# Kernel tuning notes

Measured on AMD Instinct MI355X. Metric: run time of the kernel, lower is better.

Reference implementation:

```python
import jax, jax.numpy as jnp
import numpy as np


def setup_inputs() -> dict:
    key = jax.random.key(0)
    ks = jax.random.split(key, 5)
    B, DEC, ENC, H = 4, 256, 256, 512  # feature_dim = hl_size = 512, mlp hidden = 512
    decoder_states = jax.random.normal(ks[0], (B, DEC, H), dtype=jnp.float32)
    encoder_states = jax.random.normal(ks[1], (B, ENC, H), dtype=jnp.float32)
    ext_mask = jnp.zeros((B, DEC, ENC), dtype=bool)  # self.mask set externally; all-False here
    W_mlp = jax.random.normal(ks[2], (2 * H, H), dtype=jnp.float32) * 0.02  # Linear(2H -> H)
    b_mlp = jnp.zeros((H,), dtype=jnp.float32)
    W_out = jax.random.normal(ks[3], (H, 1), dtype=jnp.float32) * 0.02  # Linear(H -> 1)
    b_out = jnp.zeros((1,), dtype=jnp.float32)
    return {"decoder_states": decoder_states, "encoder_states": encoder_states,
            "ext_mask": ext_mask, "W_mlp": W_mlp, "b_mlp": b_mlp,
            "W_out": W_out, "b_out": b_out}


def reference(decoder_states, encoder_states, ext_mask, W_mlp, b_mlp, W_out, b_out):
    # decoder_states: [B, dec, H]; encoder_states: [B, enc, H]
    H = encoder_states.shape[-1]
    # pad mask: positions where encoder feature-0 equals 0.0 -> [B, 1, enc]
    pad_mask = (encoder_states == 0.0)[:, :, :1]
    pad_mask = jnp.swapaxes(pad_mask, 1, 2)  # [B, 1, enc]
    # cat(enc, dec) @ W_mlp  ==  enc @ W_mlp[:H] + dec @ W_mlp[H:]  (avoids 2H concat)
    enc_proj = jnp.einsum('beh,hm->bem', encoder_states, W_mlp[:H])   # [B, enc, Hm]
    dec_proj = jnp.einsum('bdh,hm->bdm', decoder_states, W_mlp[H:])   # [B, dec, Hm]
    hidden = jnp.tanh(dec_proj[:, :, None, :] + enc_proj[:, None, :, :] + b_mlp)  # [B, dec, enc, Hm]
    attn = jnp.einsum('bdem,mo->bde', hidden, W_out) + b_out[0]       # [B, dec, enc]
    attn = jnp.where(ext_mask, -jnp.inf, attn)
    attn = jnp.where(pad_mask, -jnp.inf, attn)
    attn = jax.nn.softmax(attn, axis=-1)
    context = jnp.einsum('bde,beh->bdh', attn, encoder_states)        # [B, dec, H]
    return (context, attn)
```

## Files before the change

kernel.cpp:

```cpp
#include <hip/hip_runtime.h>
#include <math.h>

#define B 4
#define DEC 256
#define ENC 256
#define HDIM 512

#define TANH_SCALE 2.8853900817779268f
#define LOG2E 1.4426950408889634f

__device__ __forceinline__ float fast_exp2(float x) { return __builtin_amdgcn_exp2f(x); }
__device__ __forceinline__ float fast_rcp(float x)  { return __builtin_amdgcn_rcpf(x); }

typedef __attribute__((ext_vector_type(8))) short bf16x8;
typedef __attribute__((ext_vector_type(4))) short bf16x4;
typedef __attribute__((ext_vector_type(4))) float f32x4;

__device__ __forceinline__ unsigned short bf16_rne(float x) {
    unsigned u = __float_as_uint(x);
    return (unsigned short)((u + 0x7FFFu + ((u >> 16) & 1u)) >> 16);
}
__device__ __forceinline__ float bf16_to_f(unsigned short h) {
    return __uint_as_float((unsigned)h << 16);
}

#define W_OFS(m, k) ((((long)(m) >> 4) << 13) + (((long)(k) >> 3) << 7) + (((m) & 15) << 3) + ((k) & 7))

__global__ __launch_bounds__(256) void convert_kernel(
    const float* __restrict__ enc, const float* __restrict__ dec,
    const float* __restrict__ Wmlp,
    unsigned short* __restrict__ Xh_e, unsigned short* __restrict__ Xl_e,
    unsigned short* __restrict__ Xh_d, unsigned short* __restrict__ Xl_d,
    unsigned short* __restrict__ Wh_e, unsigned short* __restrict__ Wl_e,
    unsigned short* __restrict__ Wh_d, unsigned short* __restrict__ Wl_d)
{
    const int tid = threadIdx.x, z = blockIdx.z;
    if (z < 2) {
        const float* X = z ? dec : enc;
        unsigned short* H = z ? Xh_d : Xh_e;
        unsigned short* L = z ? Xl_d : Xl_e;
        const long i8 = ((long)blockIdx.x * 256 + tid) * 8;
        float4 v0 = *(const float4*)(X + i8);
        float4 v1 = *(const float4*)(X + i8 + 4);
        float xs[8] = {v0.x, v0.y, v0.z, v0.w, v1.x, v1.y, v1.z, v1.w};
        bf16x8 hv, lv;
#pragma unroll
        for (int j = 0; j < 8; ++j) {
            unsigned short h = bf16_rne(xs[j]);
            hv[j] = (short)h;
            lv[j] = (short)bf16_rne(xs[j] - bf16_to_f(h));
        }
        *(bf16x8*)(H + i8) = hv;
        *(bf16x8*)(L + i8) = lv;
    } else {
        const float* Wsrc = Wmlp + (z == 3 ? (long)HDIM * HDIM : 0);
        unsigned short* H = (z == 3) ? Wh_d : Wh_e;
        unsigned short* L = (z == 3) ? Wl_d : Wl_e;
        const int t = blockIdx.x * 256 + tid;
        const int m = t & 511;
        const int k0 = (t >> 9) << 2;
        bf16x4 hv, lv;
#pragma unroll
        for (int j = 0; j < 4; ++j) {
            float x = Wsrc[(long)(k0 + j) * 512 + m];
            unsigned short h = bf16_rne(x);
            hv[j] = (short)h;
            lv[j] = (short)bf16_rne(x - bf16_to_f(h));
        }
        const long ofs = W_OFS(m, k0);
        *(bf16x4*)(H + ofs) = hv;
        *(bf16x4*)(L + ofs) = lv;
    }
}

__global__ __launch_bounds__(256) void proj_mfma_kernel(
    const unsigned short* __restrict__ Xh_e, const unsigned short* __restrict__ Xl_e,
    const unsigned short* __restrict__ Xh_d, const unsigned short* __restrict__ Xl_d,
    const unsigned short* __restrict__ Wh_e, const unsigned short* __restrict__ Wl_e,
    const unsigned short* __restrict__ Wh_d, const unsigned short* __restrict__ Wl_d,
    const float* __restrict__ bmlp,
    float* __restrict__ ET, float* __restrict__ Dmat)
{
    const int tid = threadIdx.x;
    const int wave = tid >> 6, lane = tid & 63;
    const int z = blockIdx.z;
    const int r0w = blockIdx.x * 64 + wave * 16;
    const int m0 = blockIdx.y * 32;
    const unsigned short* Xh = z ? Xh_d : Xh_e;
    const unsigned short* Xl = z ? Xl_d : Xl_e;
    const unsigned short* Wh = z ? Wh_d : Wh_e;
    const unsigned short* Wl = z ? Wl_d : Wl_e;

    const int col = lane & 15;
    const int quad = lane >> 4;

    const unsigned short* pah = Xh + (long)(r0w + col) * 512 + quad * 8;
    const unsigned short* pal = Xl + (long)(r0w + col) * 512 + quad * 8;
    const long bofs = ((long)(m0 >> 4) << 13) + (quad << 7) + (col << 3);
    const unsigned short* pb0h = Wh + bofs;
    const unsigned short* pb0l = Wl + bofs;
    const unsigned short* pb1h = Wh + bofs + 8192;
    const unsigned short* pb1l = Wl + bofs + 8192;

    f32x4 a0h = {0.f,0.f,0.f,0.f}, a0x = {0.f,0.f,0.f,0.f};
    f32x4 a1h = {0.f,0.f,0.f,0.f}, a1x = {0.f,0.f,0.f,0.f};

    bf16x8 Ah = *(const bf16x8*)pah,  Al = *(const bf16x8*)pal;
    bf16x8 B0h = *(const bf16x8*)pb0h, B0l = *(const bf16x8*)pb0l;
    bf16x8 B1h = *(const bf16x8*)pb1h, B1l = *(const bf16x8*)pb1l;

#pragma unroll 1
    for (int k0 = 0; k0 < 512; k0 += 32) {
        bf16x8 nAh = Ah, nAl = Al, nB0h = B0h, nB0l = B0l, nB1h = B1h, nB1l = B1l;
        if (k0 + 32 < 512) {
            nAh = *(const bf16x8*)(pah + k0 + 32);
            nAl = *(const bf16x8*)(pal + k0 + 32);
            const long ko = (long)(k0 + 32) << 4;
            nB0h = *(const bf16x8*)(pb0h + ko);
            nB0l = *(const bf16x8*)(pb0l + ko);
            nB1h = *(const bf16x8*)(pb1h + ko);
            nB1l = *(const bf16x8*)(pb1l + ko);
        }
        a0h = __builtin_amdgcn_mfma_f32_16x16x32_bf16(Ah, B0h, a0h, 0, 0, 0);
        a1h = __builtin_amdgcn_mfma_f32_16x16x32_bf16(Ah, B1h, a1h, 0, 0, 0);
        a0x = __builtin_amdgcn_mfma_f32_16x16x32_bf16(Ah, B0l, a0x, 0, 0, 0);
        a1x = __builtin_amdgcn_mfma_f32_16x16x32_bf16(Ah, B1l, a1x, 0, 0, 0);
        a0x = __builtin_amdgcn_mfma_f32_16x16x32_bf16(Al, B0h, a0x, 0, 0, 0);
        a1x = __builtin_amdgcn_mfma_f32_16x16x32_bf16(Al, B1h, a1x, 0, 0, 0);
        Ah = nAh; Al = nAl; B0h = nB0h; B0l = nB0l; B1h = nB1h; B1l = nB1l;
    }

    if (z == 0) {
        const int batch = r0w >> 8;
        const int e0 = (r0w & 255) + quad * 4;
        float* base = ET + (long)batch * HDIM * ENC;
        float4 v;
        v.x = fast_exp2((a0h[0] + a0x[0]) * TANH_SCALE);
        v.y = fast_exp2((a0h[1] + a0x[1]) * TANH_SCALE);
        v.z = fast_exp2((a0h[2] + a0x[2]) * TANH_SCALE);
        v.w = fast_exp2((a0h[3] + a0x[3]) * TANH_SCALE);
        *(float4*)&base[(long)(m0 + col) * ENC + e0] = v;
        v.x = fast_exp2((a1h[0] + a1x[0]) * TANH_SCALE);
        v.y = fast_exp2((a1h[1] + a1x[1]) * TANH_SCALE);
        v.z = fast_exp2((a1h[2] + a1x[2]) * TANH_SCALE);
        v.w = fast_exp2((a1h[3] + a1x[3]) * TANH_SCALE);
        *(float4*)&base[(long)(m0 + 16 + col) * ENC + e0] = v;
    } else {
        const float bq0 = bmlp[m0 + col];
        const float bq1 = bmlp[m0 + 16 + col];
        const int r = r0w + quad * 4;
#pragma unroll
        for (int i = 0; i < 4; ++i) {
            Dmat[(long)(r + i) * HDIM + m0 + col] =
                fast_exp2((a0h[i] + a0x[i] + bq0) * TANH_SCALE);
            Dmat[(long)(r + i) * HDIM + m0 + 16 + col] =
                fast_exp2((a1h[i] + a1x[i] + bq1) * TANH_SCALE);
        }
    }
}

__global__ __launch_bounds__(512) void attn_ctx_kernel(
    const float* __restrict__ Dmat, const float* __restrict__ ET,
    const float* __restrict__ wo,
    const float* __restrict__ enc, const unsigned char* __restrict__ extm,
    float* __restrict__ attn_out, float* __restrict__ ctx)
{
    __shared__ __align__(16) float ds[4][HDIM];
    __shared__ __align__(16) float wos[HDIM];
    __shared__ __align__(16) float pbuf[8][4][ENC];
    __shared__ __align__(16) float as4T[ENC][4];
    __shared__ float redm[4][4];
    __shared__ float reds[4][4];

    const int tid = threadIdx.x;
    const int b = blockIdx.z, d0 = blockIdx.x * 4;
    const long g0 = (long)b * DEC + d0;
    const int rot = blockIdx.x >> 3;

    ((float4*)ds)[tid] = ((const float4*)(Dmat + g0 * HDIM))[tid];
    if (tid < 128) ((float4*)wos)[tid] = ((const float4*)wo)[tid];

    const int mg = ((tid >> 6) + rot) & 7;
    const int e4 = (tid & 63) * 4;
    const int mbase = mg * 64;
    const float* ep = ET + (long)b * HDIM * ENC + (long)mbase * ENC + e4;

    float4 rb[8];
#pragma unroll
    for (int j = 0; j < 8; ++j) rb[j] = *(const float4*)(ep + (long)j * ENC);
    __syncthreads();

    float acc[4][4] = {};
    for (int i = 0; i < 64; i += 4) {
        float4 c0 = rb[0], c1 = rb[1], c2 = rb[2], c3 = rb[3];
        rb[0] = rb[4]; rb[1] = rb[5]; rb[2] = rb[6]; rb[3] = rb[7];
        if (i + 8 < 64) {
#pragma unroll
            for (int j = 0; j < 4; ++j)
                rb[4 + j] = *(const float4*)(ep + (long)(i + 8 + j) * ENC);
        }
        const int m = mbase + i;
        const float4 w4 = *(const float4*)&wos[m];
#pragma unroll
        for (int r = 0; r < 4; ++r) {
            const float4 d4 = *(const float4*)&ds[r][m];
#pragma unroll
            for (int j = 0; j < 4; ++j) {
                acc[r][j] = fmaf(w4.x, fast_rcp(fmaf(((const float*)&c0)[j], d4.x, 1.0f)), acc[r][j]);
                acc[r][j] = fmaf(w4.y, fast_rcp(fmaf(((const float*)&c1)[j], d4.y, 1.0f)), acc[r][j]);
                acc[r][j] = fmaf(w4.z, fast_rcp(fmaf(((const float*)&c2)[j], d4.z, 1.0f)), acc[r][j]);
                acc[r][j] = fmaf(w4.w, fast_rcp(fmaf(((const float*)&c3)[j], d4.w, 1.0f)), acc[r][j]);
            }
        }
    }
#pragma unroll
    for (int r = 0; r < 4; ++r) {
        float4 v = make_float4(acc[r][0], acc[r][1], acc[r][2], acc[r][3]);
        *(float4*)&pbuf[mg][r][e4] = v;
    }
    __syncthreads();

    const int ty = tid >> 8;
    const int e = tid & 255;
    const int wave = tid >> 6, lane = tid & 63;

    const bool pad = (enc[((long)b * ENC + e) * HDIM] == 0.0f);
    float l[2], p[2];
#pragma unroll
    for (int rl = 0; rl < 2; ++rl) {
        const int r = ty * 2 + rl;
        float a = 0.f;
#pragma unroll
        for (int q = 0; q < 8; ++q) a += pbuf[q][r][e];
        const bool xm = extm[(g0 + r) * ENC + e] != 0;
        l[rl] = (pad || xm) ? -__builtin_inff() : -2.0f * a;
    }
    float mx[2] = {l[0], l[1]};
#pragma unroll
    for (int off = 32; off >= 1; off >>= 1) {
#pragma unroll
        for (int rl = 0; rl < 2; ++rl)
            mx[rl] = fmaxf(mx[rl], __shfl_xor(mx[rl], off, 64));
    }
    if (lane == 0) {
        redm[ty * 2 + 0][wave & 3] = mx[0];
        redm[ty * 2 + 1][wave & 3] = mx[1];
    }
    __syncthreads();
    float s[2];
#pragma unroll
    for (int rl = 0; rl < 2; ++rl) {
        const int r = ty * 2 + rl;
        const float gm = fmaxf(fmaxf(redm[r][0], redm[r][1]),
                               fmaxf(redm[r][2], redm[r][3]));
        p[rl] = fast_exp2((l[rl] - gm) * LOG2E);
        s[rl] = p[rl];
    }
#pragma unroll
    for (int off = 32; off >= 1; off >>= 1) {
#pragma unroll
        for (int rl = 0; rl < 2; ++rl)
            s[rl] += __shfl_xor(s[rl], off, 64);
    }
    if (lane == 0) {
        reds[ty * 2 + 0][wave & 3] = s[0];
        reds[ty * 2 + 1][wave & 3] = s[1];
    }
    __syncthreads();
#pragma unroll
    for (int rl = 0; rl < 2; ++rl) {
        const int r = ty * 2 + rl;
        const float gs = reds[r][0] + reds[r][1] + reds[r][2] + reds[r][3];
        const float pr = p[rl] * fast_rcp(gs);
        attn_out[(g0 + r) * ENC + e] = pr;
        as4T[e][r] = pr;
    }
    __syncthreads();

    float (*p4c)[4][HDIM] = (float (*)[4][HDIM])pbuf;

    const int hq = (tid & 127) * 4;
    const int eq = ((tid >> 7) + rot) & 3;
    const int ebase = eq * 64;
    const float* ew = enc + (long)b * ENC * HDIM + (long)ebase * HDIM + hq;

    float4 wb[8];
#pragma unroll
    for (int j = 0; j < 8; ++j) wb[j] = *(const float4*)(ew + (long)j * HDIM);

    float a4[4][4] = {};
    for (int i = 0; i < 64; i += 4) {
        float4 c0 = wb[0], c1 = wb[1], c2 = wb[2], c3 = wb[3];
        wb[0] = wb[4]; wb[1] = wb[5]; wb[2] = wb[6]; wb[3] = wb[7];
        if (i + 8 < 64) {
#pragma unroll
            for (int j = 0; j < 4; ++j)
                wb[4 + j] = *(const float4*)(ew + (long)(i + 8 + j) * HDIM);
        }
        float4 pa = *(const float4*)&as4T[ebase + i][0];
        float4 pb = *(const float4*)&as4T[ebase + i + 1][0];
        float4 pc = *(const float4*)&as4T[ebase + i + 2][0];
        float4 pd = *(const float4*)&as4T[ebase + i + 3][0];
#pragma unroll
        for (int r = 0; r < 4; ++r) {
            const float par = ((const float*)&pa)[r];
            const float pbr = ((const float*)&pb)[r];
            const float pcr = ((const float*)&pc)[r];
            const float pdr = ((const float*)&pd)[r];
#pragma unroll
            for (int j = 0; j < 4; ++j) {
                a4[r][j] = fmaf(par, ((const float*)&c0)[j], a4[r][j]);
                a4[r][j] = fmaf(pbr, ((const float*)&c1)[j], a4[r][j]);
                a4[r][j] = fmaf(pcr, ((const float*)&c2)[j], a4[r][j]);
                a4[r][j] = fmaf(pdr, ((const float*)&c3)[j], a4[r][j]);
            }
        }
    }
#pragma unroll
    for (int r = 0; r < 4; ++r)
        *(float4*)&p4c[eq][r][hq] = make_float4(a4[r][0], a4[r][1], a4[r][2], a4[r][3]);
    __syncthreads();

    const int h = tid;
#pragma unroll
    for (int r = 0; r < 4; ++r) {
        const float o = p4c[0][r][h] + p4c[1][r][h] + p4c[2][r][h] + p4c[3][r][h];
        ctx[(g0 + r) * HDIM + h] = o;
    }
}

extern "C" void kernel_launch(void* const* d_in, const int* in_sizes, int n_in,
                              void* d_out, int out_size, void* d_ws, size_t ws_size,
                              hipStream_t stream) {
    const float* dec = (const float*)d_in[0];
    const float* enc = (const float*)d_in[1];
    const unsigned char* extm = (const unsigned char*)d_in[2];
    const float* Wmlp = (const float*)d_in[3];
    const float* bmlp = (const float*)d_in[4];
    const float* Wout = (const float*)d_in[5];

    float* ctx = (float*)d_out;
    float* attn = ctx + (size_t)B * DEC * HDIM;

    const size_t F = (size_t)B * DEC * HDIM;
    float* ET = (float*)d_ws;
    float* Dmat = ET + F;
    unsigned short* Xh_e = (unsigned short*)(Dmat + F);
    unsigned short* Xl_e = Xh_e + F;
    unsigned short* Xh_d = Xl_e + F;
    unsigned short* Xl_d = Xh_d + F;
    unsigned short* Wh_e = Xl_d + F;
    unsigned short* Wl_e = Wh_e + HDIM * HDIM;
    unsigned short* Wh_d = Wl_e + HDIM * HDIM;
    unsigned short* Wl_d = Wh_d + HDIM * HDIM;

    convert_kernel<<<dim3(256, 1, 4), 256, 0, stream>>>(
        enc, dec, Wmlp, Xh_e, Xl_e, Xh_d, Xl_d, Wh_e, Wl_e, Wh_d, Wl_d);
    proj_mfma_kernel<<<dim3(16, 16, 2), 256, 0, stream>>>(
        Xh_e, Xl_e, Xh_d, Xl_d, Wh_e, Wl_e, Wh_d, Wl_d, bmlp, ET, Dmat);
    attn_ctx_kernel<<<dim3(DEC / 4, 1, B), 512, 0, stream>>>(
        Dmat, ET, Wout, enc, extm, attn, ctx);
}
```

Before: 108.4 us.

## Fuse convert, projection and attention kernels into one cooperative kernel

Merges the three launches (bf16 split conversion, MFMA projection, attention/softmax/context) into a single cooperative kernel of 256 blocks by 512 threads, separated by grid-wide syncs. Work of each former kernel is remapped onto the fixed block count: the conversion does two items per thread, and the projection packs two old 256-thread tiles per block. The goal is to remove launch gaps between kernels. In exchange it adds grid-sync overhead, and the projection phase now runs on 256 blocks of 512 threads instead of 512 blocks of 256.

```diff
diff --git a/kernel.cpp b/kernel.cpp
--- a/kernel.cpp
+++ b/kernel.cpp
@@ -1,5 +1,8 @@
 #include <hip/hip_runtime.h>
+#include <hip/hip_cooperative_groups.h>
 #include <math.h>
+
+namespace cg = cooperative_groups;
 
 #define B 4
 #define DEC 256
@@ -26,143 +29,15 @@
 
 #define W_OFS(m, k) ((((long)(m) >> 4) << 13) + (((long)(k) >> 3) << 7) + (((m) & 15) << 3) + ((k) & 7))
 
-__global__ __launch_bounds__(256) void convert_kernel(
+__global__ __launch_bounds__(512) void fused_kernel(
     const float* __restrict__ enc, const float* __restrict__ dec,
-    const float* __restrict__ Wmlp,
+    const float* __restrict__ Wmlp, const float* __restrict__ bmlp,
+    const float* __restrict__ wo, const unsigned char* __restrict__ extm,
     unsigned short* __restrict__ Xh_e, unsigned short* __restrict__ Xl_e,
     unsigned short* __restrict__ Xh_d, unsigned short* __restrict__ Xl_d,
     unsigned short* __restrict__ Wh_e, unsigned short* __restrict__ Wl_e,
-    unsigned short* __restrict__ Wh_d, unsigned short* __restrict__ Wl_d)
-{
-    const int tid = threadIdx.x, z = blockIdx.z;
-    if (z < 2) {
-        const float* X = z ? dec : enc;
-        unsigned short* H = z ? Xh_d : Xh_e;
-        unsigned short* L = z ? Xl_d : Xl_e;
-        const long i8 = ((long)blockIdx.x * 256 + tid) * 8;
-        float4 v0 = *(const float4*)(X + i8);
-        float4 v1 = *(const float4*)(X + i8 + 4);
-        float xs[8] = {v0.x, v0.y, v0.z, v0.w, v1.x, v1.y, v1.z, v1.w};
-        bf16x8 hv, lv;
-#pragma unroll
-        for (int j = 0; j < 8; ++j) {
-            unsigned short h = bf16_rne(xs[j]);
-            hv[j] = (short)h;
-            lv[j] = (short)bf16_rne(xs[j] - bf16_to_f(h));
-        }
-        *(bf16x8*)(H + i8) = hv;
-        *(bf16x8*)(L + i8) = lv;
-    } else {
-        const float* Wsrc = Wmlp + (z == 3 ? (long)HDIM * HDIM : 0);
-        unsigned short* H = (z == 3) ? Wh_d : Wh_e;
-        unsigned short* L = (z == 3) ? Wl_d : Wl_e;
-        const int t = blockIdx.x * 256 + tid;
-        const int m = t & 511;
-        const int k0 = (t >> 9) << 2;
-        bf16x4 hv, lv;
-#pragma unroll
-        for (int j = 0; j < 4; ++j) {
-            float x = Wsrc[(long)(k0 + j) * 512 + m];
-            unsigned short h = bf16_rne(x);
-            hv[j] = (short)h;
-            lv[j] = (short)bf16_rne(x - bf16_to_f(h));
-        }
-        const long ofs = W_OFS(m, k0);
-        *(bf16x4*)(H + ofs) = hv;
-        *(bf16x4*)(L + ofs) = lv;
-    }
-}
-
-__global__ __launch_bounds__(256) void proj_mfma_kernel(
-    const unsigned short* __restrict__ Xh_e, const unsigned short* __restrict__ Xl_e,
-    const unsigned short* __restrict__ Xh_d, const unsigned short* __restrict__ Xl_d,
-    const unsigned short* __restrict__ Wh_e, const unsigned short* __restrict__ Wl_e,
-    const unsigned short* __restrict__ Wh_d, const unsigned short* __restrict__ Wl_d,
-    const float* __restrict__ bmlp,
-    float* __restrict__ ET, float* __restrict__ Dmat)
-{
-    const int tid = threadIdx.x;
-    const int wave = tid >> 6, lane = tid & 63;
-    const int z = blockIdx.z;
-    const int r0w = blockIdx.x * 64 + wave * 16;
-    const int m0 = blockIdx.y * 32;
-    const unsigned short* Xh = z ? Xh_d : Xh_e;
-    const unsigned short* Xl = z ? Xl_d : Xl_e;
-    const unsigned short* Wh = z ? Wh_d : Wh_e;
-    const unsigned short* Wl = z ? Wl_d : Wl_e;
-
-    const int col = lane & 15;
-    const int quad = lane >> 4;
-
-    const unsigned short* pah = Xh + (long)(r0w + col) * 512 + quad * 8;
-    const unsigned short* pal = Xl + (long)(r0w + col) * 512 + quad * 8;
-    const long bofs = ((long)(m0 >> 4) << 13) + (quad << 7) + (col << 3);
-    const unsigned short* pb0h = Wh + bofs;
-    const unsigned short* pb0l = Wl + bofs;
-    const unsigned short* pb1h = Wh + bofs + 8192;
-    const unsigned short* pb1l = Wl + bofs + 8192;
-
-    f32x4 a0h = {0.f,0.f,0.f,0.f}, a0x = {0.f,0.f,0.f,0.f};
-    f32x4 a1h = {0.f,0.f,0.f,0.f}, a1x = {0.f,0.f,0.f,0.f};
-
-    bf16x8 Ah = *(const bf16x8*)pah,  Al = *(const bf16x8*)pal;
-    bf16x8 B0h = *(const bf16x8*)pb0h, B0l = *(const bf16x8*)pb0l;
-    bf16x8 B1h = *(const bf16x8*)pb1h, B1l = *(const bf16x8*)pb1l;
-
-#pragma unroll 1
-    for (int k0 = 0; k0 < 512; k0 += 32) {
-        bf16x8 nAh = Ah, nAl = Al, nB0h = B0h, nB0l = B0l, nB1h = B1h, nB1l = B1l;
-        if (k0 + 32 < 512) {
-            nAh = *(const bf16x8*)(pah + k0 + 32);
-            nAl = *(const bf16x8*)(pal + k0 + 32);
-            const long ko = (long)(k0 + 32) << 4;
-            nB0h = *(const bf16x8*)(pb0h + ko);
-            nB0l = *(const bf16x8*)(pb0l + ko);
-            nB1h = *(const bf16x8*)(pb1h + ko);
-            nB1l = *(const bf16x8*)(pb1l + ko);
-        }
-        a0h = __builtin_amdgcn_mfma_f32_16x16x32_bf16(Ah, B0h, a0h, 0, 0, 0);
-        a1h = __builtin_amdgcn_mfma_f32_16x16x32_bf16(Ah, B1h, a1h, 0, 0, 0);
-        a0x = __builtin_amdgcn_mfma_f32_16x16x32_bf16(Ah, B0l, a0x, 0, 0, 0);
-        a1x = __builtin_amdgcn_mfma_f32_16x16x32_bf16(Ah, B1l, a1x, 0, 0, 0);
-        a0x = __builtin_amdgcn_mfma_f32_16x16x32_bf16(Al, B0h, a0x, 0, 0, 0);
-        a1x = __builtin_amdgcn_mfma_f32_16x16x32_bf16(Al, B1h, a1x, 0, 0, 0);
-        Ah = nAh; Al = nAl; B0h = nB0h; B0l = nB0l; B1h = nB1h; B1l = nB1l;
-    }
-
-    if (z == 0) {
-        const int batch = r0w >> 8;
-        const int e0 = (r0w & 255) + quad * 4;
-        float* base = ET + (long)batch * HDIM * ENC;
-        float4 v;
-        v.x = fast_exp2((a0h[0] + a0x[0]) * TANH_SCALE);
-        v.y = fast_exp2((a0h[1] + a0x[1]) * TANH_SCALE);
-        v.z = fast_exp2((a0h[2] + a0x[2]) * TANH_SCALE);
-        v.w = fast_exp2((a0h[3] + a0x[3]) * TANH_SCALE);
-        *(float4*)&base[(long)(m0 + col) * ENC + e0] = v;
-        v.x = fast_exp2((a1h[0] + a1x[0]) * TANH_SCALE);
-        v.y = fast_exp2((a1h[1] + a1x[1]) * TANH_SCALE);
-        v.z = fast_exp2((a1h[2] + a1x[2]) * TANH_SCALE);
-        v.w = fast_exp2((a1h[3] + a1x[3]) * TANH_SCALE);
-        *(float4*)&base[(long)(m0 + 16 + col) * ENC + e0] = v;
-    } else {
-        const float bq0 = bmlp[m0 + col];
-        const float bq1 = bmlp[m0 + 16 + col];
-        const int r = r0w + quad * 4;
-#pragma unroll
-        for (int i = 0; i < 4; ++i) {
-            Dmat[(long)(r + i) * HDIM + m0 + col] =
-                fast_exp2((a0h[i] + a0x[i] + bq0) * TANH_SCALE);
-            Dmat[(long)(r + i) * HDIM + m0 + 16 + col] =
-                fast_exp2((a1h[i] + a1x[i] + bq1) * TANH_SCALE);
-        }
-    }
-}
-
-__global__ __launch_bounds__(512) void attn_ctx_kernel(
-    const float* __restrict__ Dmat, const float* __restrict__ ET,
-    const float* __restrict__ wo,
-    const float* __restrict__ enc, const unsigned char* __restrict__ extm,
+    unsigned short* __restrict__ Wh_d, unsigned short* __restrict__ Wl_d,
+    float* __restrict__ ET, float* __restrict__ Dmat,
     float* __restrict__ attn_out, float* __restrict__ ctx)
 {
     __shared__ __align__(16) float ds[4][HDIM];
@@ -172,160 +47,296 @@
     __shared__ float redm[4][4];
     __shared__ float reds[4][4];
 
+    cg::grid_group grid = cg::this_grid();
     const int tid = threadIdx.x;
-    const int b = blockIdx.z, d0 = blockIdx.x * 4;
-    const long g0 = (long)b * DEC + d0;
-    const int rot = blockIdx.x >> 3;
-
-    ((float4*)ds)[tid] = ((const float4*)(Dmat + g0 * HDIM))[tid];
-    if (tid < 128) ((float4*)wos)[tid] = ((const float4*)wo)[tid];
-
-    const int mg = ((tid >> 6) + rot) & 7;
-    const int e4 = (tid & 63) * 4;
-    const int mbase = mg * 64;
-    const float* ep = ET + (long)b * HDIM * ENC + (long)mbase * ENC + e4;
-
-    float4 rb[8];
-#pragma unroll
-    for (int j = 0; j < 8; ++j) rb[j] = *(const float4*)(ep + (long)j * ENC);
-    __syncthreads();
-
-    float acc[4][4] = {};
-    for (int i = 0; i < 64; i += 4) {
-        float4 c0 = rb[0], c1 = rb[1], c2 = rb[2], c3 = rb[3];
-        rb[0] = rb[4]; rb[1] = rb[5]; rb[2] = rb[6]; rb[3] = rb[7];
-        if (i + 8 < 64) {
-#pragma unroll
-            for (int j = 0; j < 4; ++j)
-                rb[4 + j] = *(const float4*)(ep + (long)(i + 8 + j) * ENC);
-        }
-        const int m = mbase + i;
-        const float4 w4 = *(const float4*)&wos[m];
+
+    {
+        const int t = blockIdx.x * 512 + tid;
+#pragma unroll
+        for (int u = 0; u < 2; ++u) {
+            const int g = t + u * 131072;
+            const int z = g >> 16;
+            const int w = g & 0xFFFF;
+            if (z < 2) {
+                const float* X = z ? dec : enc;
+                unsigned short* H = z ? Xh_d : Xh_e;
+                unsigned short* L = z ? Xl_d : Xl_e;
+                const long i8 = (long)w * 8;
+                float4 v0 = *(const float4*)(X + i8);
+                float4 v1 = *(const float4*)(X + i8 + 4);
+                float xs[8] = {v0.x, v0.y, v0.z, v0.w, v1.x, v1.y, v1.z, v1.w};
+                bf16x8 hv, lv;
+#pragma unroll
+                for (int j = 0; j < 8; ++j) {
+                    unsigned short h = bf16_rne(xs[j]);
+                    hv[j] = (short)h;
+                    lv[j] = (short)bf16_rne(xs[j] - bf16_to_f(h));
+                }
+                *(bf16x8*)(H + i8) = hv;
+                *(bf16x8*)(L + i8) = lv;
+            } else {
+                const float* Wsrc = Wmlp + (z == 3 ? (long)HDIM * HDIM : 0);
+                unsigned short* H = (z == 3) ? Wh_d : Wh_e;
+                unsigned short* L = (z == 3) ? Wl_d : Wl_e;
+                const int m = w & 511;
+                const int k0 = (w >> 9) << 2;
+                bf16x4 hv, lv;
+#pragma unroll
+                for (int j = 0; j < 4; ++j) {
+                    float x = Wsrc[(long)(k0 + j) * 512 + m];
+                    unsigned short h = bf16_rne(x);
+                    hv[j] = (short)h;
+                    lv[j] = (short)bf16_rne(x - bf16_to_f(h));
+                }
+                const long ofs = W_OFS(m, k0);
+                *(bf16x4*)(H + ofs) = hv;
+                *(bf16x4*)(L + ofs) = lv;
+            }
+        }
+    }
+    __threadfence();
+    grid.sync();
+
+    {
+        const int wave8 = tid >> 6, lane = tid & 63;
+        const int P = blockIdx.x * 2 + (wave8 >> 2);
+        const int wv = wave8 & 3;
+        const int bx = P & 15, by = (P >> 4) & 15, z = P >> 8;
+        const int r0w = bx * 64 + wv * 16;
+        const int m0 = by * 32;
+        const unsigned short* Xh = z ? Xh_d : Xh_e;
+        const unsigned short* Xl = z ? Xl_d : Xl_e;
+        const unsigned short* Wh = z ? Wh_d : Wh_e;
+        const unsigned short* Wl = z ? Wl_d : Wl_e;
+
+        const int col = lane & 15;
+        const int quad = lane >> 4;
+
+        const unsigned short* pah = Xh + (long)(r0w + col) * 512 + quad * 8;
+        const unsigned short* pal = Xl + (long)(r0w + col) * 512 + quad * 8;
+        const long bofs = ((long)(m0 >> 4) << 13) + (quad << 7) + (col << 3);
+        const unsigned short* pb0h = Wh + bofs;
+        const unsigned short* pb0l = Wl + bofs;
+        const unsigned short* pb1h = Wh + bofs + 8192;
+        const unsigned short* pb1l = Wl + bofs + 8192;
+
+        f32x4 a0h = {0.f,0.f,0.f,0.f}, a0x = {0.f,0.f,0.f,0.f};
+        f32x4 a1h = {0.f,0.f,0.f,0.f}, a1x = {0.f,0.f,0.f,0.f};
+
+        bf16x8 Ah = *(const bf16x8*)pah,  Al = *(const bf16x8*)pal;
+        bf16x8 B0h = *(const bf16x8*)pb0h, B0l = *(const bf16x8*)pb0l;
+        bf16x8 B1h = *(const bf16x8*)pb1h, B1l = *(const bf16x8*)pb1l;
+
+#pragma unroll 1
+        for (int k0 = 0; k0 < 512; k0 += 32) {
+            bf16x8 nAh = Ah, nAl = Al, nB0h = B0h, nB0l = B0l, nB1h = B1h, nB1l = B1l;
+            if (k0 + 32 < 512) {
+                nAh = *(const bf16x8*)(pah + k0 + 32);
+                nAl = *(const bf16x8*)(pal + k0 + 32);
+                const long ko = (long)(k0 + 32) << 4;
+                nB0h = *(const bf16x8*)(pb0h + ko);
+                nB0l = *(const bf16x8*)(pb0l + ko);
+                nB1h = *(const bf16x8*)(pb1h + ko);
+                nB1l = *(const bf16x8*)(pb1l + ko);
+            }
+            a0h = __builtin_amdgcn_mfma_f32_16x16x32_bf16(Ah, B0h, a0h, 0, 0, 0);
+            a1h = __builtin_amdgcn_mfma_f32_16x16x32_bf16(Ah, B1h, a1h, 0, 0, 0);
+            a0x = __builtin_amdgcn_mfma_f32_16x16x32_bf16(Ah, B0l, a0x, 0, 0, 0);
+            a1x = __builtin_amdgcn_mfma_f32_16x16x32_bf16(Ah, B1l, a1x, 0, 0, 0);
+            a0x = __builtin_amdgcn_mfma_f32_16x16x32_bf16(Al, B0h, a0x, 0, 0, 0);
+            a1x = __builtin_amdgcn_mfma_f32_16x16x32_bf16(Al, B1h, a1x, 0, 0, 0);
+            Ah = nAh; Al = nAl; B0h = nB0h; B0l = nB0l; B1h = nB1h; B1l = nB1l;
+        }
+
+        if (z == 0) {
+            const int batch = r0w >> 8;
+            const int e0 = (r0w & 255) + quad * 4;
+            float* base = ET + (long)batch * HDIM * ENC;
+            float4 v;
+            v.x = fast_exp2((a0h[0] + a0x[0]) * TANH_SCALE);
+            v.y = fast_exp2((a0h[1] + a0x[1]) * TANH_SCALE);
+            v.z = fast_exp2((a0h[2] + a0x[2]) * TANH_SCALE);
+            v.w = fast_exp2((a0h[3] + a0x[3]) * TANH_SCALE);
+            *(float4*)&base[(long)(m0 + col) * ENC + e0] = v;
+            v.x = fast_exp2((a1h[0] + a1x[0]) * TANH_SCALE);
+            v.y = fast_exp2((a1h[1] + a1x[1]) * TANH_SCALE);
+            v.z = fast_exp2((a1h[2] + a1x[2]) * TANH_SCALE);
+            v.w = fast_exp2((a1h[3] + a1x[3]) * TANH_SCALE);
+            *(float4*)&base[(long)(m0 + 16 + col) * ENC + e0] = v;
+        } else {
+            const float bq0 = bmlp[m0 + col];
+            const float bq1 = bmlp[m0 + 16 + col];
+            const int r = r0w + quad * 4;
+#pragma unroll
+            for (int i = 0; i < 4; ++i) {
+                Dmat[(long)(r + i) * HDIM + m0 + col] =
+                    fast_exp2((a0h[i] + a0x[i] + bq0) * TANH_SCALE);
+                Dmat[(long)(r + i) * HDIM + m0 + 16 + col] =
+                    fast_exp2((a1h[i] + a1x[i] + bq1) * TANH_SCALE);
+            }
+        }
+    }
+    __threadfence();
+    grid.sync();
+
+    {
+        const int bidx = blockIdx.x;
+        const int b = bidx >> 6;
+        const int dblk = bidx & 63;
+        const int d0 = dblk * 4;
+        const long g0 = (long)b * DEC + d0;
+        const int rot = dblk >> 3;
+
+        ((float4*)ds)[tid] = ((const float4*)(Dmat + g0 * HDIM))[tid];
+        if (tid < 128) ((float4*)wos)[tid] = ((const float4*)wo)[tid];
+
+        const int mg = ((tid >> 6) + rot) & 7;
+        const int e4 = (tid & 63) * 4;
+        const int mbase = mg * 64;
+        const float* ep = ET + (long)b * HDIM * ENC + (long)mbase * ENC + e4;
+
+        float4 rb[8];
+#pragma unroll
+        for (int j = 0; j < 8; ++j) rb[j] = *(const float4*)(ep + (long)j * ENC);
+        __syncthreads();
+
+        float acc[4][4] = {};
+        for (int i = 0; i < 64; i += 4) {
+            float4 c0 = rb[0], c1 = rb[1], c2 = rb[2], c3 = rb[3];
+            rb[0] = rb[4]; rb[1] = rb[5]; rb[2] = rb[6]; rb[3] = rb[7];
+            if (i + 8 < 64) {
+#pragma unroll
+                for (int j = 0; j < 4; ++j)
+                    rb[4 + j] = *(const float4*)(ep + (long)(i + 8 + j) * ENC);
+            }
+            const int m = mbase + i;
+            const float4 w4 = *(const float4*)&wos[m];
+#pragma unroll
+            for (int r = 0; r < 4; ++r) {
+                const float4 d4 = *(const float4*)&ds[r][m];
+#pragma unroll
+                for (int j = 0; j < 4; ++j) {
+                    acc[r][j] = fmaf(w4.x, fast_rcp(fmaf(((const float*)&c0)[j], d4.x, 1.0f)), acc[r][j]);
+                    acc[r][j] = fmaf(w4.y, fast_rcp(fmaf(((const float*)&c1)[j], d4.y, 1.0f)), acc[r][j]);
+                    acc[r][j] = fmaf(w4.z, fast_rcp(fmaf(((const float*)&c2)[j], d4.z, 1.0f)), acc[r][j]);
+                    acc[r][j] = fmaf(w4.w, fast_rcp(fmaf(((const float*)&c3)[j], d4.w, 1.0f)), acc[r][j]);
+                }
+            }
+        }
 #pragma unroll
         for (int r = 0; r < 4; ++r) {
-            const float4 d4 = *(const float4*)&ds[r][m];
-#pragma unroll
-            for (int j = 0; j < 4; ++j) {
-                acc[r][j] = fmaf(w4.x, fast_rcp(fmaf(((const float*)&c0)[j], d4.x, 1.0f)), acc[r][j]);
-                acc[r][j] = fmaf(w4.y, fast_rcp(fmaf(((const float*)&c1)[j], d4.y, 1.0f)), acc[r][j]);
-                acc[r][j] = fmaf(w4.z, fast_rcp(fmaf(((const float*)&c2)[j], d4.z, 1.0f)), acc[r][j]);
-                acc[r][j] = fmaf(w4.w, fast_rcp(fmaf(((const float*)&c3)[j], d4.w, 1.0f)), acc[r][j]);
-            }
-        }
-    }
-#pragma unroll
-    for (int r = 0; r < 4; ++r) {
-        float4 v = make_float4(acc[r][0], acc[r][1], acc[r][2], acc[r][3]);
-        *(float4*)&pbuf[mg][r][e4] = v;
-    }
-    __syncthreads();
-
-    const int ty = tid >> 8;
-    const int e = tid & 255;
-    const int wave = tid >> 6, lane = tid & 63;
-
-    const bool pad = (enc[((long)b * ENC + e) * HDIM] == 0.0f);
-    float l[2], p[2];
-#pragma unroll
-    for (int rl = 0; rl < 2; ++rl) {
-        const int r = ty * 2 + rl;
-        float a = 0.f;
-#pragma unroll
-        for (int q = 0; q < 8; ++q) a += pbuf[q][r][e];
-        const bool xm = extm[(g0 + r) * ENC + e] != 0;
-        l[rl] = (pad || xm) ? -__builtin_inff() : -2.0f * a;
-    }
-    float mx[2] = {l[0], l[1]};
-#pragma unroll
-    for (int off = 32; off >= 1; off >>= 1) {
-#pragma unroll
-        for (int rl = 0; rl < 2; ++rl)
-            mx[rl] = fmaxf(mx[rl], __shfl_xor(mx[rl], off, 64));
-    }
-    if (lane == 0) {
-        redm[ty * 2 + 0][wave & 3] = mx[0];
-        redm[ty * 2 + 1][wave & 3] = mx[1];
-    }
-    __syncthreads();
-    float s[2];
-#pragma unroll
-    for (int rl = 0; rl < 2; ++rl) {
-        const int r = ty * 2 + rl;
-        const float gm = fmaxf(fmaxf(redm[r][0], redm[r][1]),
-                               fmaxf(redm[r][2], redm[r][3]));
-        p[rl] = fast_exp2((l[rl] - gm) * LOG2E);
-        s[rl] = p[rl];
-    }
-#pragma unroll
-    for (int off = 32; off >= 1; off >>= 1) {
-#pragma unroll
-        for (int rl = 0; rl < 2; ++rl)
-            s[rl] += __shfl_xor(s[rl], off, 64);
-    }
-    if (lane == 0) {
-        reds[ty * 2 + 0][wave & 3] = s[0];
-        reds[ty * 2 + 1][wave & 3] = s[1];
-    }
-    __syncthreads();
-#pragma unroll
-    for (int rl = 0; rl < 2; ++rl) {
-        const int r = ty * 2 + rl;
-        const float gs = reds[r][0] + reds[r][1] + reds[r][2] + reds[r][3];
-        const float pr = p[rl] * fast_rcp(gs);
-        attn_out[(g0 + r) * ENC + e] = pr;
-        as4T[e][r] = pr;
-    }
-    __syncthreads();
-
-    float (*p4c)[4][HDIM] = (float (*)[4][HDIM])pbuf;
-
-    const int hq = (tid & 127) * 4;
-    const int eq = ((tid >> 7) + rot) & 3;
-    const int ebase = eq * 64;
-    const float* ew = enc + (long)b * ENC * HDIM + (long)ebase * HDIM + hq;
-
-    float4 wb[8];
-#pragma unroll
-    for (int j = 0; j < 8; ++j) wb[j] = *(const float4*)(ew + (long)j * HDIM);
-
-    float a4[4][4] = {};
-    for (int i = 0; i < 64; i += 4) {
-        float4 c0 = wb[0], c1 = wb[1], c2 = wb[2], c3 = wb[3];
-        wb[0] = wb[4]; wb[1] = wb[5]; wb[2] = wb[6]; wb[3] = wb[7];
-        if (i + 8 < 64) {
-#pragma unroll
-            for (int j = 0; j < 4; ++j)
-                wb[4 + j] = *(const float4*)(ew + (long)(i + 8 + j) * HDIM);
-        }
-        float4 pa = *(const float4*)&as4T[ebase + i][0];
-        float4 pb = *(const float4*)&as4T[ebase + i + 1][0];
-        float4 pc = *(const float4*)&as4T[ebase + i + 2][0];
-        float4 pd = *(const float4*)&as4T[ebase + i + 3][0];
+            float4 v = make_float4(acc[r][0], acc[r][1], acc[r][2], acc[r][3]);
+            *(float4*)&pbuf[mg][r][e4] = v;
+        }
+        __syncthreads();
+
+        const int ty = tid >> 8;
+        const int e = tid & 255;
+        const int wave = tid >> 6, lane = tid & 63;
+
+        const bool pad = (enc[((long)b * ENC + e) * HDIM] == 0.0f);
+        float l[2], p[2];
+#pragma unroll
+        for (int rl = 0; rl < 2; ++rl) {
+            const int r = ty * 2 + rl;
+            float a = 0.f;
+#pragma unroll
+            for (int q = 0; q < 8; ++q) a += pbuf[q][r][e];
+            const bool xm = extm[(g0 + r) * ENC + e] != 0;
+            l[rl] = (pad || xm) ? -__builtin_inff() : -2.0f * a;
+        }
+        float mx[2] = {l[0], l[1]};
+#pragma unroll
+        for (int off = 32; off >= 1; off >>= 1) {
+#pragma unroll
+            for (int rl = 0; rl < 2; ++rl)
+                mx[rl] = fmaxf(mx[rl], __shfl_xor(mx[rl], off, 64));
+        }
+        if (lane == 0) {
+            redm[ty * 2 + 0][wave & 3] = mx[0];
+            redm[ty * 2 + 1][wave & 3] = mx[1];
+        }
+        __syncthreads();
+        float s[2];
+#pragma unroll
+        for (int rl = 0; rl < 2; ++rl) {
+            const int r = ty * 2 + rl;
+            const float gm = fmaxf(fmaxf(redm[r][0], redm[r][1]),
+                                   fmaxf(redm[r][2], redm[r][3]));
+            p[rl] = fast_exp2((l[rl] - gm) * LOG2E);
+            s[rl] = p[rl];
+        }
+#pragma unroll
+        for (int off = 32; off >= 1; off >>= 1) {
+#pragma unroll
+            for (int rl = 0; rl < 2; ++rl)
+                s[rl] += __shfl_xor(s[rl], off, 64);
+        }
+        if (lane == 0) {
+            reds[ty * 2 + 0][wave & 3] = s[0];
+            reds[ty * 2 + 1][wave & 3] = s[1];
+        }
+        __syncthreads();
+#pragma unroll
+        for (int rl = 0; rl < 2; ++rl) {
+            const int r = ty * 2 + rl;
+            const float gs = reds[r][0] + reds[r][1] + reds[r][2] + reds[r][3];
+            const float pr = p[rl] * fast_rcp(gs);
+            attn_out[(g0 + r) * ENC + e] = pr;
+            as4T[e][r] = pr;
+        }
+        __syncthreads();
+
+        float (*p4c)[4][HDIM] = (float (*)[4][HDIM])pbuf;
+
+        const int hq = (tid & 127) * 4;
+        const int eq = ((tid >> 7) + rot) & 3;
+        const int ebase = eq * 64;
+        const float* ew = enc + (long)b * ENC * HDIM + (long)ebase * HDIM + hq;
+
+        float4 wb[8];
+#pragma unroll
+        for (int j = 0; j < 8; ++j) wb[j] = *(const float4*)(ew + (long)j * HDIM);
+
+        float a4[4][4] = {};
+        for (int i = 0; i < 64; i += 4) {
+            float4 c0 = wb[0], c1 = wb[1], c2 = wb[2], c3 = wb[3];
+            wb[0] = wb[4]; wb[1] = wb[5]; wb[2] = wb[6]; wb[3] = wb[7];
+            if (i + 8 < 64) {
+#pragma unroll
+                for (int j = 0; j < 4; ++j)
+                    wb[4 + j] = *(const float4*)(ew + (long)(i + 8 + j) * HDIM);
+            }
+            float4 pa = *(const float4*)&as4T[ebase + i][0];
+            float4 pb = *(const float4*)&as4T[ebase + i + 1][0];
+            float4 pc = *(const float4*)&as4T[ebase + i + 2][0];
+            float4 pd = *(const float4*)&as4T[ebase + i + 3][0];
+#pragma unroll
+            for (int r = 0; r < 4; ++r) {
+                const float par = ((const float*)&pa)[r];
+                const float pbr = ((const float*)&pb)[r];
+                const float pcr = ((const float*)&pc)[r];
+                const float pdr = ((const float*)&pd)[r];
+#pragma unroll
+                for (int j = 0; j < 4; ++j) {
+                    a4[r][j] = fmaf(par, ((const float*)&c0)[j], a4[r][j]);
+                    a4[r][j] = fmaf(pbr, ((const float*)&c1)[j], a4[r][j]);
+                    a4[r][j] = fmaf(pcr, ((const float*)&c2)[j], a4[r][j]);
+                    a4[r][j] = fmaf(pdr, ((const float*)&c3)[j], a4[r][j]);
+                }
+            }
+        }
+#pragma unroll
+        for (int r = 0; r < 4; ++r)
+            *(float4*)&p4c[eq][r][hq] = make_float4(a4[r][0], a4[r][1], a4[r][2], a4[r][3]);
+        __syncthreads();
+
+        const int h = tid;
 #pragma unroll
         for (int r = 0; r < 4; ++r) {
-            const float par = ((const float*)&pa)[r];
-            const float pbr = ((const float*)&pb)[r];
-            const float pcr = ((const float*)&pc)[r];
-            const float pdr = ((const float*)&pd)[r];
-#pragma unroll
-            for (int j = 0; j < 4; ++j) {
-                a4[r][j] = fmaf(par, ((const float*)&c0)[j], a4[r][j]);
-                a4[r][j] = fmaf(pbr, ((const float*)&c1)[j], a4[r][j]);
-                a4[r][j] = fmaf(pcr, ((const float*)&c2)[j], a4[r][j]);
-                a4[r][j] = fmaf(pdr, ((const float*)&c3)[j], a4[r][j]);
-            }
-        }
-    }
-#pragma unroll
-    for (int r = 0; r < 4; ++r)
-        *(float4*)&p4c[eq][r][hq] = make_float4(a4[r][0], a4[r][1], a4[r][2], a4[r][3]);
-    __syncthreads();
-
-    const int h = tid;
-#pragma unroll
-    for (int r = 0; r < 4; ++r) {
-        const float o = p4c[0][r][h] + p4c[1][r][h] + p4c[2][r][h] + p4c[3][r][h];
-        ctx[(g0 + r) * HDIM + h] = o;
+            const float o = p4c[0][r][h] + p4c[1][r][h] + p4c[2][r][h] + p4c[3][r][h];
+            ctx[(g0 + r) * HDIM + h] = o;
+        }
     }
 }
 
@@ -354,10 +365,12 @@
     unsigned short* Wh_d = Wl_e + HDIM * HDIM;
     unsigned short* Wl_d = Wh_d + HDIM * HDIM;
 
-    convert_kernel<<<dim3(256, 1, 4), 256, 0, stream>>>(
-        enc, dec, Wmlp, Xh_e, Xl_e, Xh_d, Xl_d, Wh_e, Wl_e, Wh_d, Wl_d);
-    proj_mfma_kernel<<<dim3(16, 16, 2), 256, 0, stream>>>(
-        Xh_e, Xl_e, Xh_d, Xl_d, Wh_e, Wl_e, Wh_d, Wl_d, bmlp, ET, Dmat);
-    attn_ctx_kernel<<<dim3(DEC / 4, 1, B), 512, 0, stream>>>(
-        Dmat, ET, Wout, enc, extm, attn, ctx);
+    void* kargs[] = {
+        (void*)&enc, (void*)&dec, (void*)&Wmlp, (void*)&bmlp,
+        (void*)&Wout, (void*)&extm,
+        (void*)&Xh_e, (void*)&Xl_e, (void*)&Xh_d, (void*)&Xl_d,
+        (void*)&Wh_e, (void*)&Wl_e, (void*)&Wh_d, (void*)&Wl_d,
+        (void*)&ET, (void*)&Dmat, (void*)&attn, (void*)&ctx};
+    hipLaunchCooperativeKernel((const void*)fused_kernel, dim3(256), dim3(512),
+                               kargs, 0, stream);
 }
```

New measurement: 285.4 us. 2.63x slower.
